# Optimization experiments

Measured on AMD Instinct MI355X. Metric: run time of the kernel, lower is better.

Reference implementation:

```python
import jax, jax.numpy as jnp
import numpy as np

B, S, DIM = 2, 2048, 1024
N_HEADS, HEAD_DIM = 16, 64
ROPE_THETA = 10000.0


def _rope_cos_sin(seq_len, head_dim, dtype=jnp.float32):
    inv_freq = 1.0 / (ROPE_THETA ** (jnp.arange(0, head_dim, 2, dtype=jnp.float32) / head_dim))
    ang = jnp.arange(seq_len, dtype=jnp.float32)[:, None] * inv_freq[None, :]  # [S, D/2]
    return jnp.cos(ang).astype(dtype), jnp.sin(ang).astype(dtype)


def _apply_rope(t, cos, sin):
    # t: [B, S, H, D]; cos/sin: [S, D/2]
    t1 = t[..., 0::2]
    t2 = t[..., 1::2]
    c = cos[None, :, None, :]
    s = sin[None, :, None, :]
    r1 = t1 * c - t2 * s
    r2 = t1 * s + t2 * c
    # interleave back to original even/odd layout
    return jnp.stack([r1, r2], axis=-1).reshape(t.shape)


def setup_inputs() -> dict:
    key = jax.random.key(0)
    ks = jax.random.split(key, 5)
    scale = 1.0 / np.sqrt(DIM)
    return {
        "x": jax.random.normal(ks[0], (B, S, DIM), dtype=jnp.float32),
        "Wq": jax.random.normal(ks[1], (DIM, DIM), dtype=jnp.float32) * scale,
        "Wk": jax.random.normal(ks[2], (DIM, DIM), dtype=jnp.float32) * scale,
        "Wv": jax.random.normal(ks[3], (DIM, DIM), dtype=jnp.float32) * scale,
        "Wo": jax.random.normal(ks[4], (DIM, DIM), dtype=jnp.float32) * scale,
    }


def reference(x, Wq, Wk, Wv, Wo):
    b, s, _ = x.shape
    q = (x @ Wq.T).reshape(b, s, N_HEADS, HEAD_DIM)
    k = (x @ Wk.T).reshape(b, s, N_HEADS, HEAD_DIM)
    v = (x @ Wv.T).reshape(b, s, N_HEADS, HEAD_DIM)

    cos, sin = _rope_cos_sin(s, HEAD_DIM, dtype=q.dtype)
    q = _apply_rope(q, cos, sin)
    k = _apply_rope(k, cos, sin)

    # [B, H, S, S] scores with causal mask
    attn = jnp.einsum("bqhd,bkhd->bhqk", q, k) / np.sqrt(HEAD_DIM)
    causal = jnp.tril(jnp.ones((s, s), dtype=bool))
    attn = jnp.where(causal[None, None], attn, jnp.float32(-jnp.inf))
    probs = jax.nn.softmax(attn.astype(jnp.float32), axis=-1).astype(q.dtype)

    out = jnp.einsum("bhqk,bkhd->bqhd", probs, v).reshape(b, s, N_HEADS * HEAD_DIM)
    return out @ Wo.T
```

## Files before the change

### kernel.cpp

```cpp
#include <hip/hip_runtime.h>
#include <hip/hip_bf16.h>

#define S_LEN 2048
#define DIMSZ 1024
#define NH    16
#define HD    64

typedef __attribute__((ext_vector_type(8))) short short8v;
typedef __attribute__((ext_vector_type(4))) short short4v;
typedef __attribute__((ext_vector_type(4))) float f32x4;

typedef const __attribute__((address_space(1))) unsigned GU;
typedef __attribute__((address_space(3))) unsigned LU;

__device__ __forceinline__ void gl16(const ushort* g, ushort* l) {
  __builtin_amdgcn_global_load_lds((GU*)g, (LU*)l, 16, 0, 0);
}

__device__ __forceinline__ ushort f2bf(float f) {
  union { float f; unsigned u; } v; v.f = f;
  unsigned u = v.u;
  return (ushort)((u + 0x7FFFu + ((u >> 16) & 1u)) >> 16);
}

__device__ __forceinline__ uint cvtpk(float lo, float hi) {
  uint d;
  asm("v_cvt_pk_bf16_f32 %0, %1, %2" : "=v"(d) : "v"(lo), "v"(hi));
  return d;
}

__global__ __launch_bounds__(256) void cvt_k(
    const float* __restrict__ x, const float* __restrict__ wq,
    const float* __restrict__ wk, const float* __restrict__ wv,
    const float* __restrict__ wo,
    ushort* __restrict__ xb, ushort* __restrict__ wqkvb, ushort* __restrict__ wob)
{
  size_t gid = (size_t)blockIdx.x * 256 + threadIdx.x;
  size_t e0 = gid * 8;
  const float* src; ushort* dst;
  if (e0 < (4u << 20)) { src = x + e0; dst = xb + e0; }
  else if (e0 < (7u << 20)) {
    size_t o = e0 - (4u << 20);
    const float* w = (o < (1u << 20)) ? wq : ((o < (2u << 20)) ? wk : wv);
    src = w + (o & ((1u << 20) - 1)); dst = wqkvb + o;
  } else {
    size_t o = e0 - (7u << 20);
    src = wo + o; dst = wob + o;
  }
  float4 a = *(const float4*)src;
  float4 b = *(const float4*)(src + 4);
  short8v h;
  h[0] = (short)f2bf(a.x); h[1] = (short)f2bf(a.y);
  h[2] = (short)f2bf(a.z); h[3] = (short)f2bf(a.w);
  h[4] = (short)f2bf(b.x); h[5] = (short)f2bf(b.y);
  h[6] = (short)f2bf(b.z); h[7] = (short)f2bf(b.w);
  *(short8v*)dst = h;
}

__global__ __launch_bounds__(256) void rope_table_k(float2* __restrict__ tab) {
  int i = blockIdx.x * 256 + threadIdx.x;
  int f = i >> 11, s = i & (S_LEN - 1);
  float inv = powf(10000.f, -(float)f * (1.f / 32.f));
  float ang = (float)s * inv;
  tab[i] = make_float2(cosf(ang), sinf(ang));
}

#define QSTAGE(c, kt_) do {                                                     \
    int k0_ = (kt_) * 64;                                                       \
    _Pragma("unroll")                                                           \
    for (int j_ = 0; j_ < 4; ++j_) {                                            \
      int R_ = w * 32 + j_ * 8;                                                 \
      gl16(xb + (size_t)(bm + R_ + r8) * DIMSZ + k0_ + cswz, &lA[c][R_ * 64]);  \
      gl16(W  + (size_t)(bn + R_ + r8) * DIMSZ + k0_ + cswz, &lB[c][R_ * 64]);  \
    }                                                                           \
  } while (0)

__global__ __launch_bounds__(256) void gemm_qkv_k(
    const ushort* __restrict__ xb, const ushort* __restrict__ wqkvb,
    ushort* __restrict__ qb, ushort* __restrict__ kb, ushort* __restrict__ vtb,
    const float2* __restrict__ rtab)
{
  __shared__ ushort lA[2][128 * 64];
  __shared__ ushort lB[2][128 * 64];
  const int t = threadIdx.x;
  int id = blockIdx.x;
  int nid = (id & 7) * 96 + (id >> 3);
  const int which = nid >> 8;
  const int bm = ((nid >> 3) & 31) * 128, bn = (nid & 7) * 128;
  const ushort* W = wqkvb + ((size_t)which << 20);
  const int w = t >> 6, l = t & 63, lr = l & 15, lg = l >> 4;
  const int wm = (w >> 1) * 64, wn = (w & 1) * 64;
  const int r8 = l >> 3;
  const int cswz = ((l & 7) ^ r8) * 8;

  f32x4 acc[4][4] = {};

  QSTAGE(0, 0);
  __syncthreads();
  for (int kt = 0; kt < DIMSZ / 64; ++kt) {
    const int cur = kt & 1;
    if (kt + 1 < DIMSZ / 64) QSTAGE(cur ^ 1, kt + 1);
    #pragma unroll
    for (int kk = 0; kk < 2; ++kk) {
      short8v a[4], b[4];
      #pragma unroll
      for (int mt = 0; mt < 4; ++mt) {
        int row = wm + mt * 16 + lr;
        a[mt] = *(const short8v*)((const char*)lA[cur] + row * 128 + ((kk * 64 + lg * 16) ^ ((row & 7) << 4)));
      }
      #pragma unroll
      for (int nt = 0; nt < 4; ++nt) {
        int row = wn + nt * 16 + lr;
        b[nt] = *(const short8v*)((const char*)lB[cur] + row * 128 + ((kk * 64 + lg * 16) ^ ((row & 7) << 4)));
      }
      #pragma unroll
      for (int mt = 0; mt < 4; ++mt)
        #pragma unroll
        for (int nt = 0; nt < 4; ++nt)
          acc[mt][nt] = __builtin_amdgcn_mfma_f32_16x16x32_bf16(b[nt], a[mt], acc[mt][nt], 0, 0, 0);
    }
    __syncthreads();
  }

  const int bb = bm >> 11, s_base = bm & (S_LEN - 1);

  if (which == 2) {
    ushort* tb = &lA[0][0];
    #pragma unroll
    for (int mt = 0; mt < 4; ++mt)
      #pragma unroll
      for (int nt = 0; nt < 4; ++nt)
        #pragma unroll
        for (int r = 0; r < 4; ++r) {
          int row = wn + nt * 16 + lg * 4 + r;
          int col = wm + mt * 16 + lr;
          int byte = row * 256 + ((col * 2) ^ (((row >> 2) & 3) << 5));
          *(ushort*)((char*)tb + byte) = f2bf(acc[mt][nt][r]);
        }
    __syncthreads();
    int row = t >> 1, half = t & 1;
    int h = (bn + row) >> 6, d = (bn + row) & 63;
    ushort* vdst = vtb + ((size_t)(bb * NH + h) * HD + d) * S_LEN + s_base + half * 64;
    #pragma unroll
    for (int j = 0; j < 8; ++j) {
      int byte = row * 256 + ((half * 128 + j * 16) ^ (((row >> 2) & 3) << 5));
      *(short8v*)(vdst + j * 8) = *(const short8v*)((const char*)tb + byte);
    }
  } else {
    ushort* dst = (which == 0) ? qb : kb;
    const float QS = (which == 0) ? (0.125f * 1.4426950408889634f) : 1.0f;
    #pragma unroll
    for (int mt = 0; mt < 4; ++mt) {
      int s = s_base + wm + mt * 16 + lr;
      #pragma unroll
      for (int nt = 0; nt < 4; ++nt) {
        int nw = bn + wn + nt * 16 + lg * 4;
        int h = nw >> 6, d0 = nw & 63;
        uint pk[2];
        #pragma unroll
        for (int rp = 0; rp < 2; ++rp) {
          float2 cs = rtab[(d0 >> 1) * S_LEN + rp * S_LEN + s];
          float t1 = acc[mt][nt][2 * rp], t2 = acc[mt][nt][2 * rp + 1];
          float o0 = (t1 * cs.x - t2 * cs.y) * QS;
          float o1 = (t1 * cs.y + t2 * cs.x) * QS;
          pk[rp] = (uint)f2bf(o0) | ((uint)f2bf(o1) << 16);
        }
        uint2 pv; pv.x = pk[0]; pv.y = pk[1];
        *(uint2*)(dst + ((size_t)(bb * NH + h) * S_LEN + s) * HD + d0) = pv;
      }
    }
  }
}

template<bool DIAG>
__device__ __forceinline__ void attn_tile(
    const ushort* lK, const ushort* lV, ushort* lPw,
    const short8v* qf, f32x4* o, float& m2, float& lsum,
    int lr, int lg, int wrow)
{
  f32x4 sacc[4] = {};
  __builtin_amdgcn_s_setprio(1);
  #pragma unroll
  for (int kk = 0; kk < 2; ++kk)
    #pragma unroll
    for (int jt = 0; jt < 4; ++jt) {
      int row = jt * 16 + lr;
      short8v kf = *(const short8v*)((const char*)lK + row * 128 + ((kk * 64 + lg * 16) ^ ((row & 7) << 4)));
      sacc[jt] = __builtin_amdgcn_mfma_f32_16x16x32_bf16(kf, qf[kk], sacc[jt], 0, 0, 0);
    }
  __builtin_amdgcn_s_setprio(0);

  float v2[4][4];
  #pragma unroll
  for (int jt = 0; jt < 4; ++jt)
    #pragma unroll
    for (int r = 0; r < 4; ++r) {
      float sv = sacc[jt][r];
      if (DIAG && (jt * 16 + lg * 4 + r > wrow + lr)) sv = -3e38f;
      v2[jt][r] = sv;
    }
  float mj[4];
  #pragma unroll
  for (int jt = 0; jt < 4; ++jt)
    mj[jt] = fmaxf(fmaxf(v2[jt][0], v2[jt][1]), fmaxf(v2[jt][2], v2[jt][3]));
  float rmax = fmaxf(fmaxf(mj[0], mj[1]), fmaxf(mj[2], mj[3]));
  rmax = fmaxf(rmax, __shfl_xor(rmax, 16));
  rmax = fmaxf(rmax, __shfl_xor(rmax, 32));

  const bool need = __any(rmax > m2 + 8.f);
  float mn = m2;
  float so = 1.f;
  if (need) {
    mn = fmaxf(m2, rmax);
    so = exp2f(m2 - mn);
    m2 = mn;
  }
  float pe[4][4];
  float ps = 0.f;
  #pragma unroll
  for (int jt = 0; jt < 4; ++jt)
    #pragma unroll
    for (int r = 0; r < 4; ++r) {
      pe[jt][r] = exp2f(v2[jt][r] - mn);
      ps += pe[jt][r];
    }
  ps += __shfl_xor(ps, 16);
  ps += __shfl_xor(ps, 32);
  if (need) {
    lsum = lsum * so + ps;
    #pragma unroll
    for (int r = 0; r < 4; ++r) {
      float sor = __shfl(so, lg * 4 + r);
      #pragma unroll
      for (int dt = 0; dt < 4; ++dt) o[dt][r] *= sor;
    }
  } else {
    lsum += ps;
  }
  #pragma unroll
  for (int jt = 0; jt < 4; ++jt) {
    uint2 pv;
    pv.x = cvtpk(pe[jt][0], pe[jt][1]);
    pv.y = cvtpk(pe[jt][2], pe[jt][3]);
    *(uint2*)((char*)lPw + lr * 128 + ((jt * 32 + lg * 8) ^ ((lr & 7) << 4))) = pv;
  }
  __builtin_amdgcn_s_setprio(1);
  #pragma unroll
  for (int kk = 0; kk < 2; ++kk) {
    short8v pa = *(const short8v*)((const char*)lPw + lr * 128 + ((kk * 64 + lg * 16) ^ ((lr & 7) << 4)));
    #pragma unroll
    for (int dt = 0; dt < 4; ++dt) {
      int row = dt * 16 + lr;
      short8v vb = *(const short8v*)((const char*)lV + row * 128 + ((kk * 64 + lg * 16) ^ ((row & 7) << 4)));
      o[dt] = __builtin_amdgcn_mfma_f32_16x16x32_bf16(pa, vb, o[dt], 0, 0, 0);
    }
  }
  __builtin_amdgcn_s_setprio(0);
}

#define ITEM_KT(i_) (((i_) <= qtB) ? (i_) : ((i_) - qtB - 1))

#define FSTAGE(c, rnd) do {                                                   \
    int i0_ = (rnd) * 2, i1_ = i0_ + 1;                                       \
    int ka_ = ITEM_KT(i0_) * 64;                                              \
    int kb_ = ((i1_ <= 32) ? ITEM_KT(i1_) : 0) * 64;                          \
    gl16(kbh + (size_t)(ka_ + trow) * HD + cswz,    &lKb[c][0][w * 512]);     \
    gl16(kbh + (size_t)(kb_ + trow) * HD + cswz,    &lKb[c][1][w * 512]);     \
    gl16(vbh + (size_t)trow * S_LEN + ka_ + cswz,   &lVb[c][0][w * 512]);     \
    gl16(vbh + (size_t)trow * S_LEN + kb_ + cswz,   &lVb[c][1][w * 512]);     \
  } while (0)

__global__ __launch_bounds__(512, 4) void flash_k(
    const ushort* __restrict__ qb, const ushort* __restrict__ kb,
    const ushort* __restrict__ vtb, ushort* __restrict__ ab)
{
  __shared__ ushort lKb[2][2][64 * 64];
  __shared__ ushort lVb[2][2][64 * 64];
  __shared__ ushort lP[8][16 * 64];

  int id = blockIdx.y * 16 + blockIdx.x;
  int nid = (id & 7) * 64 + (id >> 3);
  const int pr = nid & 15, bh = nid >> 4;
  const int qtA = pr, qtB = 31 - pr;

  const int t = threadIdx.x, w = t >> 6, l = t & 63, lr = l & 15, lg = l >> 4;
  const int g = w >> 2, ws = w & 3;
  const int r8 = l >> 3;
  const int cswz = ((l & 7) ^ r8) * 8;
  const int trow = t >> 3;
  const ushort* kbh = kb + (size_t)bh * S_LEN * HD;
  const ushort* vbh = vtb + (size_t)bh * HD * S_LEN;

  short8v qfA[2], qfB[2];
  #pragma unroll
  for (int kk = 0; kk < 2; ++kk) {
    qfA[kk] = *(const short8v*)(qb + ((size_t)bh * S_LEN + qtA * 64 + ws * 16 + lr) * HD + kk * 32 + lg * 8);
    qfB[kk] = *(const short8v*)(qb + ((size_t)bh * S_LEN + qtB * 64 + ws * 16 + lr) * HD + kk * 32 + lg * 8);
  }

  float mA = -3e38f, lsA = 0.f, mB = -3e38f, lsB = 0.f;
  f32x4 oA[4] = {}, oB[4] = {};

  FSTAGE(0, 0);
  asm volatile("s_waitcnt vmcnt(0)" ::: "memory");

  const int NR = 17;
  for (int rnd = 0; rnd < NR; ++rnd) {
    const int cur = rnd & 1;
    if (rnd + 1 < NR) {
      FSTAGE(cur ^ 1, rnd + 1);
      asm volatile("s_waitcnt vmcnt(4)" ::: "memory");
    } else {
      asm volatile("s_waitcnt vmcnt(0)" ::: "memory");
    }
    __builtin_amdgcn_s_barrier();
    asm volatile("" ::: "memory");
    const int it = 2 * rnd + g;
    if (it <= 32) {
      const ushort* lK = lKb[cur][g];
      const ushort* lV = lVb[cur][g];
      if (it <= qtB) {
        if (it == qtB) attn_tile<true >(lK, lV, lP[w], qfB, oB, mB, lsB, lr, lg, ws * 16);
        else           attn_tile<false>(lK, lV, lP[w], qfB, oB, mB, lsB, lr, lg, ws * 16);
      } else {
        const int ka = it - qtB - 1;
        if (ka == qtA) attn_tile<true >(lK, lV, lP[w], qfA, oA, mA, lsA, lr, lg, ws * 16);
        else           attn_tile<false>(lK, lV, lP[w], qfA, oA, mA, lsA, lr, lg, ws * 16);
      }
    }
    __builtin_amdgcn_s_barrier();
    asm volatile("" ::: "memory");
  }

  float* obB = (float*)&lKb[0][0][0];
  float* obA = (float*)&lVb[0][0][0];
  float* ml  = (float*)&lP[0][0];
  const int blk = g * 4 + ws;
  #pragma unroll
  for (int dt = 0; dt < 4; ++dt)
    #pragma unroll
    for (int r = 0; r < 4; ++r) {
      obB[blk * 1024 + (lg * 4 + r) * 64 + dt * 16 + lr] = oB[dt][r];
      obA[blk * 1024 + (lg * 4 + r) * 64 + dt * 16 + lr] = oA[dt][r];
    }
  if (lg == 0) {
    ml[(blk * 16 + lr) * 2 + 0] = mB;  ml[(blk * 16 + lr) * 2 + 1] = lsB;
    ml[512 + (blk * 16 + lr) * 2 + 0] = mA;  ml[512 + (blk * 16 + lr) * 2 + 1] = lsA;
  }
  __syncthreads();

  const float* mlm = ml + (g ? 512 : 0);
  const float* o0  = (g ? obA : obB) + ws * 1024;
  const float* o1  = (g ? obA : obB) + (4 + ws) * 1024;
  const int qt = g ? qtA : qtB;
  const int b = bh >> 4, h = bh & 15;
  #pragma unroll
  for (int r = 0; r < 4; ++r) {
    int row = lg * 4 + r;
    float m0 = mlm[(ws * 16 + row) * 2 + 0], l0 = mlm[(ws * 16 + row) * 2 + 1];
    float m1 = mlm[((4 + ws) * 16 + row) * 2 + 0], l1 = mlm[((4 + ws) * 16 + row) * 2 + 1];
    float msr = fmaxf(m0, m1);
    float a0 = exp2f(m0 - msr), a1 = exp2f(m1 - msr);
    float inv = 1.f / (l0 * a0 + l1 * a1);
    int qg = qt * 64 + ws * 16 + row;
    #pragma unroll
    for (int dt = 0; dt < 4; ++dt) {
      float v = o0[row * 64 + dt * 16 + lr] * a0 + o1[row * 64 + dt * 16 + lr] * a1;
      ab[((size_t)b * S_LEN + qg) * DIMSZ + h * HD + dt * 16 + lr] = f2bf(v * inv);
    }
  }
}

#define OSTAGE(c, kt_) do {                                                     \
    int k0_ = (kt_) * 64;                                                       \
    _Pragma("unroll")                                                           \
    for (int j_ = 0; j_ < 4; ++j_) {                                            \
      int R_ = w * 32 + j_ * 8;                                                 \
      gl16(ab  + (size_t)(bm + R_ + r8) * DIMSZ + k0_ + cswz, &lA[c][R_ * 64]); \
      gl16(wob + (size_t)(bn + R_ + r8) * DIMSZ + k0_ + cswz, &lB[c][R_ * 64]); \
    }                                                                           \
  } while (0)

__global__ __launch_bounds__(256) void gemm_out_k(
    const ushort* __restrict__ ab, const ushort* __restrict__ wob, float* __restrict__ out)
{
  __shared__ ushort lA[2][128 * 64];
  __shared__ ushort lB[2][128 * 64];
  const int t = threadIdx.x;
  int id = blockIdx.x;
  int nid = (id & 7) * 32 + (id >> 3);
  const int bm = (nid >> 3) * 128, bn = (nid & 7) * 128;
  const int w = t >> 6, l = t & 63, lr = l & 15, lg = l >> 4;
  const int wm = (w >> 1) * 64, wn = (w & 1) * 64;
  const int r8 = l >> 3;
  const int cswz = ((l & 7) ^ r8) * 8;

  f32x4 acc[4][4] = {};

  OSTAGE(0, 0);
  __syncthreads();
  for (int kt = 0; kt < DIMSZ / 64; ++kt) {
    const int cur = kt & 1;
    if (kt + 1 < DIMSZ / 64) OSTAGE(cur ^ 1, kt + 1);
    #pragma unroll
    for (int kk = 0; kk < 2; ++kk) {
      short8v a[4], b[4];
      #pragma unroll
      for (int mt = 0; mt < 4; ++mt) {
        int row = wm + mt * 16 + lr;
        a[mt] = *(const short8v*)((const char*)lA[cur] + row * 128 + ((kk * 64 + lg * 16) ^ ((row & 7) << 4)));
      }
      #pragma unroll
      for (int nt = 0; nt < 4; ++nt) {
        int row = wn + nt * 16 + lr;
        b[nt] = *(const short8v*)((const char*)lB[cur] + row * 128 + ((kk * 64 + lg * 16) ^ ((row & 7) << 4)));
      }
      #pragma unroll
      for (int mt = 0; mt < 4; ++mt)
        #pragma unroll
        for (int nt = 0; nt < 4; ++nt)
          acc[mt][nt] = __builtin_amdgcn_mfma_f32_16x16x32_bf16(b[nt], a[mt], acc[mt][nt], 0, 0, 0);
    }
    __syncthreads();
  }

  #pragma unroll
  for (int mt = 0; mt < 4; ++mt) {
    int m = bm + wm + mt * 16 + lr;
    #pragma unroll
    for (int nt = 0; nt < 4; ++nt) {
      int nb = bn + wn + nt * 16 + lg * 4;
      *(f32x4*)(out + (size_t)m * DIMSZ + nb) = acc[mt][nt];
    }
  }
}

extern "C" void kernel_launch(void* const* d_in, const int* in_sizes, int n_in,
                              void* d_out, int out_size, void* d_ws, size_t ws_size,
                              hipStream_t stream) {
  (void)in_sizes; (void)n_in; (void)out_size; (void)ws_size;
  const float* x  = (const float*)d_in[0];
  const float* Wq = (const float*)d_in[1];
  const float* Wk = (const float*)d_in[2];
  const float* Wv = (const float*)d_in[3];
  const float* Wo = (const float*)d_in[4];
  float* out = (float*)d_out;

  char* ws = (char*)d_ws;
  ushort* qb    = (ushort*)(ws);
  ushort* kb    = (ushort*)(ws + ((size_t)8  << 20));
  ushort* vtb   = (ushort*)(ws + ((size_t)16 << 20));
  ushort* xb    = (ushort*)(ws + ((size_t)24 << 20));
  ushort* ab    = xb;
  ushort* wqkvb = (ushort*)(ws + ((size_t)32 << 20));
  ushort* wob   = (ushort*)(ws + ((size_t)38 << 20));
  float2* rtab  = (float2*)(ws + ((size_t)40 << 20));

  hipLaunchKernelGGL(cvt_k, dim3(4096), dim3(256), 0, stream,
                     x, Wq, Wk, Wv, Wo, xb, wqkvb, wob);
  hipLaunchKernelGGL(rope_table_k, dim3(S_LEN * 32 / 256), dim3(256), 0, stream, rtab);
  hipLaunchKernelGGL(gemm_qkv_k, dim3(768), dim3(256), 0, stream,
                     xb, wqkvb, qb, kb, vtb, rtab);
  hipLaunchKernelGGL(flash_k, dim3(16, 32), dim3(512), 0, stream, qb, kb, vtb, ab);
  hipLaunchKernelGGL(gemm_out_k, dim3(256), dim3(256), 0, stream, ab, wob, out);
}
```

Measured before the change: 132.0 us.

## Load V fragments directly from global into registers, dropping V LDS staging

The flash attention kernel no longer stages V tiles through shared memory. Each wave now loads its V^T MFMA B-operand fragments straight from global memory into registers, and the per-round wait moves to after compute. This halves LDS usage, so more blocks may fit per CU and LDS traffic drops. The epilogue reduction is split into two phases so it can reuse the smaller K buffer as scratch. In exchange, global V loads now sit on each wave's critical path without async prefetch, every wave fetches its own V data redundantly, and the epilogue gains an extra barrier.

```diff
diff --git a/kernel.cpp b/kernel.cpp
--- a/kernel.cpp
+++ b/kernel.cpp
@@ -174,7 +174,7 @@
 
 template<bool DIAG>
 __device__ __forceinline__ void attn_tile(
-    const ushort* lK, const ushort* lV, ushort* lPw,
+    const ushort* lK, const short8v vr[2][4], ushort* lPw,
     const short8v* qf, f32x4* o, float& m2, float& lsum,
     int lr, int lg, int wrow)
 {
@@ -249,11 +249,8 @@
   for (int kk = 0; kk < 2; ++kk) {
     short8v pa = *(const short8v*)((const char*)lPw + lr * 128 + ((kk * 64 + lg * 16) ^ ((lr & 7) << 4)));
     #pragma unroll
-    for (int dt = 0; dt < 4; ++dt) {
-      int row = dt * 16 + lr;
-      short8v vb = *(const short8v*)((const char*)lV + row * 128 + ((kk * 64 + lg * 16) ^ ((row & 7) << 4)));
-      o[dt] = __builtin_amdgcn_mfma_f32_16x16x32_bf16(pa, vb, o[dt], 0, 0, 0);
-    }
+    for (int dt = 0; dt < 4; ++dt)
+      o[dt] = __builtin_amdgcn_mfma_f32_16x16x32_bf16(pa, vr[kk][dt], o[dt], 0, 0, 0);
   }
   __builtin_amdgcn_s_setprio(0);
 }
@@ -264,10 +261,8 @@
     int i0_ = (rnd) * 2, i1_ = i0_ + 1;                                       \
     int ka_ = ITEM_KT(i0_) * 64;                                              \
     int kb_ = ((i1_ <= 32) ? ITEM_KT(i1_) : 0) * 64;                          \
-    gl16(kbh + (size_t)(ka_ + trow) * HD + cswz,    &lKb[c][0][w * 512]);     \
-    gl16(kbh + (size_t)(kb_ + trow) * HD + cswz,    &lKb[c][1][w * 512]);     \
-    gl16(vbh + (size_t)trow * S_LEN + ka_ + cswz,   &lVb[c][0][w * 512]);     \
-    gl16(vbh + (size_t)trow * S_LEN + kb_ + cswz,   &lVb[c][1][w * 512]);     \
+    gl16(kbh + (size_t)(ka_ + trow) * HD + cswz, &lKb[c][0][w * 512]);        \
+    gl16(kbh + (size_t)(kb_ + trow) * HD + cswz, &lKb[c][1][w * 512]);        \
   } while (0)
 
 __global__ __launch_bounds__(512, 4) void flash_k(
@@ -275,7 +270,6 @@
     const ushort* __restrict__ vtb, ushort* __restrict__ ab)
 {
   __shared__ ushort lKb[2][2][64 * 64];
-  __shared__ ushort lVb[2][2][64 * 64];
   __shared__ ushort lP[8][16 * 64];
 
   int id = blockIdx.y * 16 + blockIdx.x;
@@ -303,70 +297,74 @@
 
   FSTAGE(0, 0);
   asm volatile("s_waitcnt vmcnt(0)" ::: "memory");
+  __builtin_amdgcn_s_barrier();
+  asm volatile("" ::: "memory");
 
   const int NR = 17;
   for (int rnd = 0; rnd < NR; ++rnd) {
     const int cur = rnd & 1;
-    if (rnd + 1 < NR) {
-      FSTAGE(cur ^ 1, rnd + 1);
-      asm volatile("s_waitcnt vmcnt(4)" ::: "memory");
-    } else {
-      asm volatile("s_waitcnt vmcnt(0)" ::: "memory");
-    }
+    if (rnd + 1 < NR) FSTAGE(cur ^ 1, rnd + 1);
+    const int it = 2 * rnd + g;
+    if (it <= 32) {
+      const int k0 = ITEM_KT(it) * 64;
+      short8v vr[2][4];
+      #pragma unroll
+      for (int kk = 0; kk < 2; ++kk)
+        #pragma unroll
+        for (int dt = 0; dt < 4; ++dt)
+          vr[kk][dt] = *(const short8v*)(vbh + (size_t)(dt * 16 + lr) * S_LEN + k0 + kk * 32 + lg * 8);
+      const ushort* lK = lKb[cur][g];
+      if (it <= qtB) {
+        if (it == qtB) attn_tile<true >(lK, vr, lP[w], qfB, oB, mB, lsB, lr, lg, ws * 16);
+        else           attn_tile<false>(lK, vr, lP[w], qfB, oB, mB, lsB, lr, lg, ws * 16);
+      } else {
+        if (it == 32) attn_tile<true >(lK, vr, lP[w], qfA, oA, mA, lsA, lr, lg, ws * 16);
+        else          attn_tile<false>(lK, vr, lP[w], qfA, oA, mA, lsA, lr, lg, ws * 16);
+      }
+    }
+    asm volatile("s_waitcnt vmcnt(0)" ::: "memory");
     __builtin_amdgcn_s_barrier();
     asm volatile("" ::: "memory");
-    const int it = 2 * rnd + g;
-    if (it <= 32) {
-      const ushort* lK = lKb[cur][g];
-      const ushort* lV = lVb[cur][g];
-      if (it <= qtB) {
-        if (it == qtB) attn_tile<true >(lK, lV, lP[w], qfB, oB, mB, lsB, lr, lg, ws * 16);
-        else           attn_tile<false>(lK, lV, lP[w], qfB, oB, mB, lsB, lr, lg, ws * 16);
-      } else {
-        const int ka = it - qtB - 1;
-        if (ka == qtA) attn_tile<true >(lK, lV, lP[w], qfA, oA, mA, lsA, lr, lg, ws * 16);
-        else           attn_tile<false>(lK, lV, lP[w], qfA, oA, mA, lsA, lr, lg, ws * 16);
-      }
-    }
-    __builtin_amdgcn_s_barrier();
-    asm volatile("" ::: "memory");
-  }
-
-  float* obB = (float*)&lKb[0][0][0];
-  float* obA = (float*)&lVb[0][0][0];
-  float* ml  = (float*)&lP[0][0];
+  }
+
+  float* scratch = (float*)&lKb[0][0][0];
+  float* ml = (float*)&lP[0][0];
   const int blk = g * 4 + ws;
-  #pragma unroll
-  for (int dt = 0; dt < 4; ++dt)
-    #pragma unroll
-    for (int r = 0; r < 4; ++r) {
-      obB[blk * 1024 + (lg * 4 + r) * 64 + dt * 16 + lr] = oB[dt][r];
-      obA[blk * 1024 + (lg * 4 + r) * 64 + dt * 16 + lr] = oA[dt][r];
-    }
-  if (lg == 0) {
-    ml[(blk * 16 + lr) * 2 + 0] = mB;  ml[(blk * 16 + lr) * 2 + 1] = lsB;
-    ml[512 + (blk * 16 + lr) * 2 + 0] = mA;  ml[512 + (blk * 16 + lr) * 2 + 1] = lsA;
-  }
-  __syncthreads();
-
-  const float* mlm = ml + (g ? 512 : 0);
-  const float* o0  = (g ? obA : obB) + ws * 1024;
-  const float* o1  = (g ? obA : obB) + (4 + ws) * 1024;
-  const int qt = g ? qtA : qtB;
   const int b = bh >> 4, h = bh & 15;
   #pragma unroll
-  for (int r = 0; r < 4; ++r) {
-    int row = lg * 4 + r;
-    float m0 = mlm[(ws * 16 + row) * 2 + 0], l0 = mlm[(ws * 16 + row) * 2 + 1];
-    float m1 = mlm[((4 + ws) * 16 + row) * 2 + 0], l1 = mlm[((4 + ws) * 16 + row) * 2 + 1];
-    float msr = fmaxf(m0, m1);
-    float a0 = exp2f(m0 - msr), a1 = exp2f(m1 - msr);
-    float inv = 1.f / (l0 * a0 + l1 * a1);
-    int qg = qt * 64 + ws * 16 + row;
-    #pragma unroll
-    for (int dt = 0; dt < 4; ++dt) {
-      float v = o0[row * 64 + dt * 16 + lr] * a0 + o1[row * 64 + dt * 16 + lr] * a1;
-      ab[((size_t)b * S_LEN + qg) * DIMSZ + h * HD + dt * 16 + lr] = f2bf(v * inv);
+  for (int phase = 0; phase < 2; ++phase) {
+    const f32x4* om = phase ? oA : oB;
+    float mm = phase ? mA : mB;
+    float ll = phase ? lsA : lsB;
+    __syncthreads();
+    #pragma unroll
+    for (int dt = 0; dt < 4; ++dt)
+      #pragma unroll
+      for (int r = 0; r < 4; ++r)
+        scratch[blk * 1024 + (lg * 4 + r) * 64 + dt * 16 + lr] = om[dt][r];
+    if (lg == 0) {
+      ml[(blk * 16 + lr) * 2 + 0] = mm;
+      ml[(blk * 16 + lr) * 2 + 1] = ll;
+    }
+    __syncthreads();
+    if (g == phase) {
+      const int qt = phase ? qtA : qtB;
+      #pragma unroll
+      for (int r = 0; r < 4; ++r) {
+        int row = lg * 4 + r;
+        float m0 = ml[(ws * 16 + row) * 2 + 0],       l0 = ml[(ws * 16 + row) * 2 + 1];
+        float m1 = ml[((4 + ws) * 16 + row) * 2 + 0], l1 = ml[((4 + ws) * 16 + row) * 2 + 1];
+        float msr = fmaxf(m0, m1);
+        float a0 = exp2f(m0 - msr), a1 = exp2f(m1 - msr);
+        float inv = 1.f / (l0 * a0 + l1 * a1);
+        int qg = qt * 64 + ws * 16 + row;
+        #pragma unroll
+        for (int dt = 0; dt < 4; ++dt) {
+          float v = scratch[ws * 1024 + row * 64 + dt * 16 + lr] * a0
+                  + scratch[(4 + ws) * 1024 + row * 64 + dt * 16 + lr] * a1;
+          ab[((size_t)b * S_LEN + qg) * DIMSZ + h * HD + dt * 16 + lr] = f2bf(v * inv);
+        }
+      }
     }
   }
 }
```

Result: slower. 229.3 us (+73.7%).
